# Kernel optimization log

Hardware: AMD Instinct MI355X
Metric: run time of the kernel (lower is better)

## Reference

```python
import jax, jax.numpy as jnp
import numpy as np

B = 64      # graphs in data1 batch
K = 50      # SortAggregation k
NPG = 1600  # nodes per graph in data1 (equal-size, contiguous batch vector)


def gcn_layer(x, src, dst, ew, W, b):
    # PyG GCNConv with edge_weight: add self loops (weight 1), symmetric norm.
    n = x.shape[0]
    idx = jnp.arange(n)
    src2 = jnp.concatenate([src, idx])
    dst2 = jnp.concatenate([dst, idx])
    ew2 = jnp.concatenate([ew, jnp.ones((n,), x.dtype)])
    deg = jax.ops.segment_sum(ew2, dst2, num_segments=n)
    dinv = jnp.where(deg > 0, jax.lax.rsqrt(deg), 0.0)
    norm = dinv[src2] * ew2 * dinv[dst2]
    h = x @ W                                   # [n, out]
    out = jax.ops.segment_sum(h[src2] * norm[:, None], dst2, num_segments=n)
    return out + b


def gnn(x, ei, ew, Wg1, bg1, Wg2, bg2):
    src, dst = ei[0], ei[1]
    h = jax.nn.relu(gcn_layer(x, src, dst, ew, Wg1, bg1))
    return jax.nn.relu(gcn_layer(h, src, dst, ew, Wg2, bg2))


def layer_norm(x, g, b, eps=1e-5):
    m = jnp.mean(x, -1, keepdims=True)
    v = jnp.mean((x - m) ** 2, -1, keepdims=True)
    return (x - m) * jax.lax.rsqrt(v + eps) * g + b


def setup_inputs() -> dict:
    key = jax.random.key(0)
    ks = jax.random.split(key, 16)
    N1, N2, F, E1, E2 = B * NPG, 199, 128, 1638400, 3184
    s = 0.05
    inp = {}
    inp["x1"] = jax.random.normal(ks[0], (N1, F), jnp.float32)
    inp["edge_attr1"] = jax.random.uniform(ks[1], (E1,), jnp.float32)
    inp["x2"] = jax.random.normal(ks[2], (N2, F), jnp.float32)
    inp["edge_attr2"] = jax.random.uniform(ks[3], (E2,), jnp.float32)
    inp["Wg1"] = jax.random.normal(ks[4], (F, 128), jnp.float32) * s
    inp["bg1"] = jnp.zeros((128,), jnp.float32)
    inp["Wg2"] = jax.random.normal(ks[5], (128, 64), jnp.float32) * s
    inp["bg2"] = jnp.zeros((64,), jnp.float32)
    inp["fc1_W"] = jax.random.normal(ks[6], (K * N2, 128), jnp.float32) * s
    inp["fc1_b"] = jnp.zeros((128,), jnp.float32)
    inp["ln1_g"] = jnp.ones((128,), jnp.float32)
    inp["ln1_b"] = jnp.zeros((128,), jnp.float32)
    inp["fc2_W"] = jax.random.normal(ks[7], (128, 64), jnp.float32) * s
    inp["fc2_b"] = jnp.zeros((64,), jnp.float32)
    inp["ln2_g"] = jnp.ones((64,), jnp.float32)
    inp["ln2_b"] = jnp.zeros((64,), jnp.float32)
    inp["fc3_W"] = jax.random.normal(ks[8], (64, 1), jnp.float32) * s
    inp["fc3_b"] = jnp.zeros((1,), jnp.float32)
    inp["edge_index1"] = jax.random.randint(ks[9], (2, E1), 0, N1)
    inp["edge_index2"] = jax.random.randint(ks[10], (2, E2), 0, N2)
    inp["batch1"] = jnp.repeat(jnp.arange(B), NPG)
    return inp


def reference(x1, edge_attr1, x2, edge_attr2, Wg1, bg1, Wg2, bg2,
              fc1_W, fc1_b, ln1_g, ln1_b, fc2_W, fc2_b, ln2_g, ln2_b,
              fc3_W, fc3_b, edge_index1, edge_index2, batch1):
    o1 = gnn(x1, edge_index1, edge_attr1, Wg1, bg1, Wg2, bg2)   # [N1, 64]
    o2 = gnn(x2, edge_index2, edge_attr2, Wg1, bg1, Wg2, bg2)   # [N2, 64]
    # torch.cdist(p=2) via gram trick (stable sqrt)
    d2 = (jnp.sum(o1 * o1, 1)[:, None] + jnp.sum(o2 * o2, 1)[None, :]
          - 2.0 * (o1 @ o2.T))
    dist = jnp.sqrt(jnp.maximum(d2, 0.0) + 1e-12)               # [N1, N2]
    # SortAggregation: batch1 is contiguous with equal-size graphs -> reshape
    dense = dist.reshape(B, NPG, -1)                            # [B, NPG, N2]
    _, idx = jax.lax.top_k(dense[:, :, -1], K)   # sort desc by last channel
    pooled = jnp.take_along_axis(dense, idx[:, :, None], axis=1)  # [B, K, N2]
    h = pooled.reshape(B, -1) @ fc1_W + fc1_b                   # [B, 128]
    h = jax.nn.relu(layer_norm(h, ln1_g, ln1_b))
    h = jax.nn.relu(layer_norm(h @ fc2_W + fc2_b, ln2_g, ln2_b))
    return jax.nn.sigmoid(h @ fc3_W + fc3_b)                    # [B, 1]
```

## Files before the change

### kernel.cpp

```cpp
#include <hip/hip_runtime.h>
#include <hip/hip_bf16.h>
#include <cstdint>


__device__ __forceinline__ int rfl(int v) { return __builtin_amdgcn_readfirstlane(v); }

__device__ __forceinline__ unsigned short f2bf(float f) {
    unsigned u = __float_as_uint(f);
    u = (u + 0x7fffu + ((u >> 16) & 1u)) >> 16;
    return (unsigned short)u;
}
__device__ __forceinline__ float lo16(unsigned v) { return __uint_as_float(v << 16); }
__device__ __forceinline__ float hi16(unsigned v) { return __uint_as_float(v & 0xffff0000u); }

#define BSHIFT 7
#define BNODES 128
#define BCAP 3072
#define XPAD 65

__global__ void bhist_kernel(const int* __restrict__ dst, int* bcnt, int E, int nbuk) {
    __shared__ int bins[832];
    int t = threadIdx.x;
    for (int i = t; i < nbuk; i += 256) bins[i] = 0;
    __syncthreads();
    for (int e = blockIdx.x * 256 + t; e < E; e += gridDim.x * 256)
        atomicAdd(&bins[dst[e] >> BSHIFT], 1);
    __syncthreads();
    for (int i = t; i < nbuk; i += 256) {
        int v = bins[i];
        if (v) atomicAdd(&bcnt[i], v);
    }
}

__global__ void bscan_kernel(const int* __restrict__ bcnt, int* __restrict__ boff,
                             int* __restrict__ bcur, int* __restrict__ off,
                             int nbuk, int E, int N1) {
    __shared__ int carry_s;
    int lane = threadIdx.x;
    if (lane == 0) carry_s = 0;
    __syncthreads();
    for (int base = 0; base < nbuk; base += 64) {
        int i = base + lane;
        int v = (i < nbuk) ? bcnt[i] : 0;
        int s = v;
        for (int d2 = 1; d2 < 64; d2 <<= 1) { int u = __shfl_up(s, d2); if (lane >= d2) s += u; }
        int c = carry_s;
        if (i < nbuk) { boff[i] = c + s - v; bcur[i] = c + s - v; }
        __syncthreads();
        if (lane == 63) carry_s = c + s;
        __syncthreads();
    }
    if (lane == 0) { boff[nbuk] = E; off[N1] = E; }
}

#define BP_EPB 16384
__global__ __launch_bounds__(1024) void bpart_kernel(const int* __restrict__ dst,
                                                     const int* __restrict__ src,
                                                     const float* __restrict__ ew,
                                                     int* bcur, int2* __restrict__ stag,
                                                     int E, int nbuk) {
    __shared__ int cnt[832];
    __shared__ int base[832];
    int t = threadIdx.x;
    int e0 = blockIdx.x * BP_EPB;
    for (int i = t; i < nbuk; i += 1024) cnt[i] = 0;
    __syncthreads();
#pragma unroll
    for (int k = 0; k < 16; k++) {
        int e = e0 + k * 1024 + t;
        if (e < E) atomicAdd(&cnt[dst[e] >> BSHIFT], 1);
    }
    __syncthreads();
    for (int i = t; i < nbuk; i += 1024) {
        int c = cnt[i];
        base[i] = c ? atomicAdd(&bcur[i], c) : 0;
    }
    __syncthreads();
    for (int i = t; i < nbuk; i += 1024) cnt[i] = 0;
    __syncthreads();
#pragma unroll
    for (int k = 0; k < 16; k++) {
        int e = e0 + k * 1024 + t;
        if (e < E) {
            int d = dst[e];
            int b = d >> BSHIFT, dl = d & (BNODES - 1);
            int l = atomicAdd(&cnt[b], 1);
            stag[base[b] + l] = make_int2((src[e] & 0xFFFFF) | (dl << 20),
                                          __float_as_int(ew[e]));
        }
    }
}

__global__ __launch_bounds__(256) void bfine_kernel(const int2* __restrict__ stag,
                                                    const int* __restrict__ boff,
                                                    int2* __restrict__ packed,
                                                    int* __restrict__ off,
                                                    float* __restrict__ dinv,
                                                    int nbuk, int N1) {
    __shared__ int2 ein[BCAP];
    __shared__ int2 eout[BCAP];
    __shared__ float ews[BNODES];
    __shared__ int hist[BNODES];
    __shared__ int sb[BNODES];
    __shared__ int cnt2[BNODES];
    int b = blockIdx.x, t = threadIdx.x;
    int base = boff[b], nE = boff[b + 1] - base;
    bool staged = (nE <= BCAP);
    if (t < BNODES) { hist[t] = 0; ews[t] = 0.f; cnt2[t] = 0; }
    __syncthreads();
    if (staged)
        for (int i = t; i < nE; i += 256) ein[i] = stag[base + i];
    __syncthreads();
    for (int i = t; i < nE; i += 256) {
        int2 m = staged ? ein[i] : stag[base + i];
        int dl = m.x >> 20;
        atomicAdd(&hist[dl], 1);
        atomicAdd(&ews[dl], __int_as_float(m.y));
    }
    __syncthreads();
    if (t < 64) {
        int v0 = hist[t]; int s0 = v0;
        for (int d2 = 1; d2 < 64; d2 <<= 1) { int u = __shfl_up(s0, d2); if (t >= d2) s0 += u; }
        sb[t] = s0 - v0;
        int tot0 = __shfl(s0, 63);
        int v1 = hist[64 + t]; int s1 = v1;
        for (int d2 = 1; d2 < 64; d2 <<= 1) { int u = __shfl_up(s1, d2); if (t >= d2) s1 += u; }
        sb[64 + t] = tot0 + s1 - v1;
    }
    __syncthreads();
    int node = b * BNODES + t;
    if (t < BNODES && node < N1) {
        off[node] = base + sb[t];
        dinv[node] = rsqrtf(1.0f + ews[t]);
    }
    __syncthreads();
    for (int i = t; i < nE; i += 256) {
        int2 m = staged ? ein[i] : stag[base + i];
        int dl = m.x >> 20;
        int l = atomicAdd(&cnt2[dl], 1);
        int2 o = make_int2(m.x & 0xFFFFF, m.y);
        if (staged) eout[sb[dl] + l] = o;
        else packed[base + sb[dl] + l] = o;
    }
    __syncthreads();
    if (staged)
        for (int i = t; i < nE; i += 256) packed[base + i] = eout[i];
}

__global__ __launch_bounds__(256) void gemm128_kernel(const float* __restrict__ x,
                                                      const float* __restrict__ w,
                                                      const float* __restrict__ dinv,
                                                      unsigned short* __restrict__ outb,
                                                      int nrows) {
    __shared__ float ws[64 * 128];
    __shared__ float xs[64 * XPAD];
    int t = threadIdx.x;
    size_t r0 = (size_t)blockIdx.x * 64;
    int tx = t % 16, ty = t / 16;
    float acc[4][8];
#pragma unroll
    for (int i = 0; i < 4; i++)
#pragma unroll
        for (int j = 0; j < 8; j++) acc[i][j] = 0.f;

    for (int half = 0; half < 2; half++) {
        __syncthreads();
        for (int f = t; f < 64 * 32; f += 256)
            ((float4*)ws)[f] = ((const float4*)(w + half * 64 * 128))[f];
        for (int f = t; f < 64 * 16; f += 256) {
            int row = f >> 4, c4 = f & 15;
            float4 v = *((const float4*)(x + (r0 + row) * 128 + half * 64 + c4 * 4));
            xs[row * XPAD + c4 * 4]     = v.x;
            xs[row * XPAD + c4 * 4 + 1] = v.y;
            xs[row * XPAD + c4 * 4 + 2] = v.z;
            xs[row * XPAD + c4 * 4 + 3] = v.w;
        }
        __syncthreads();
        for (int k = 0; k < 64; k++) {
            float4 b0 = *((const float4*)(ws + k * 128 + tx * 4));
            float4 b1 = *((const float4*)(ws + k * 128 + 64 + tx * 4));
            float bb[8] = {b0.x, b0.y, b0.z, b0.w, b1.x, b1.y, b1.z, b1.w};
#pragma unroll
            for (int i = 0; i < 4; i++) {
                float a = xs[(ty * 4 + i) * XPAD + k];
#pragma unroll
                for (int j = 0; j < 8; j++) acc[i][j] = fmaf(a, bb[j], acc[i][j]);
            }
        }
    }
#pragma unroll
    for (int i = 0; i < 4; i++) {
        size_t row = r0 + ty * 4 + i;
        float dv = dinv[row];
        uint2 pkA, pkB;
        pkA.x = (unsigned)f2bf(acc[i][0] * dv) | ((unsigned)f2bf(acc[i][1] * dv) << 16);
        pkA.y = (unsigned)f2bf(acc[i][2] * dv) | ((unsigned)f2bf(acc[i][3] * dv) << 16);
        pkB.x = (unsigned)f2bf(acc[i][4] * dv) | ((unsigned)f2bf(acc[i][5] * dv) << 16);
        pkB.y = (unsigned)f2bf(acc[i][6] * dv) | ((unsigned)f2bf(acc[i][7] * dv) << 16);
        *((uint2*)(outb + row * 128 + tx * 4)) = pkA;
        *((uint2*)(outb + row * 128 + 64 + tx * 4)) = pkB;
    }
}

__global__ __launch_bounds__(256) void gemm64b_kernel(const float* __restrict__ x,
                                                      const float* __restrict__ w,
                                                      const float* __restrict__ dinv,
                                                      unsigned short* __restrict__ outb,
                                                      int nrows) {
    __shared__ float ws[64 * 64];
    __shared__ float xs[64 * XPAD];
    int t = threadIdx.x;
    size_t r0 = (size_t)blockIdx.x * 64;
    int tx = t % 8, ty = t / 8;
    float acc[2][8];
#pragma unroll
    for (int i = 0; i < 2; i++)
#pragma unroll
        for (int j = 0; j < 8; j++) acc[i][j] = 0.f;

    for (int half = 0; half < 2; half++) {
        __syncthreads();
        for (int f = t; f < 64 * 16; f += 256)
            ((float4*)ws)[f] = ((const float4*)(w + half * 64 * 64))[f];
        for (int f = t; f < 64 * 16; f += 256) {
            int row = f >> 4, c4 = f & 15;
            float4 v = *((const float4*)(x + (r0 + row) * 128 + half * 64 + c4 * 4));
            xs[row * XPAD + c4 * 4]     = v.x;
            xs[row * XPAD + c4 * 4 + 1] = v.y;
            xs[row * XPAD + c4 * 4 + 2] = v.z;
            xs[row * XPAD + c4 * 4 + 3] = v.w;
        }
        __syncthreads();
        for (int k = 0; k < 64; k++) {
            float4 b0 = *((const float4*)(ws + k * 64 + tx * 4));
            float4 b1 = *((const float4*)(ws + k * 64 + 32 + tx * 4));
            float bb[8] = {b0.x, b0.y, b0.z, b0.w, b1.x, b1.y, b1.z, b1.w};
#pragma unroll
            for (int i = 0; i < 2; i++) {
                float a = xs[(ty * 2 + i) * XPAD + k];
#pragma unroll
                for (int j = 0; j < 8; j++) acc[i][j] = fmaf(a, bb[j], acc[i][j]);
            }
        }
    }
#pragma unroll
    for (int i = 0; i < 2; i++) {
        size_t row = r0 + ty * 2 + i;
        float dv = dinv[row];
        uint2 pk;
        pk.x = (unsigned)f2bf(acc[i][0] * dv) | ((unsigned)f2bf(acc[i][1] * dv) << 16);
        pk.y = (unsigned)f2bf(acc[i][2] * dv) | ((unsigned)f2bf(acc[i][3] * dv) << 16);
        *((uint2*)(outb + row * 64 + tx * 4)) = pk;
        pk.x = (unsigned)f2bf(acc[i][4] * dv) | ((unsigned)f2bf(acc[i][5] * dv) << 16);
        pk.y = (unsigned)f2bf(acc[i][6] * dv) | ((unsigned)f2bf(acc[i][7] * dv) << 16);
        *((uint2*)(outb + row * 64 + 32 + tx * 4)) = pk;
    }
}

__global__ __launch_bounds__(256) void agg128_kernel(const unsigned short* __restrict__ zs,
                                                     const int2* __restrict__ packed,
                                                     const int* __restrict__ off,
                                                     const float* __restrict__ dinv,
                                                     const float* __restrict__ bias,
                                                     float* __restrict__ h, int n) {
    int wid = threadIdx.x >> 6;
    int lane = threadIdx.x & 63;
    int d = rfl(blockIdx.x * 4 + wid);
    if (d >= n) return;
    const unsigned short* zl = zs + lane * 2;
    float dv = dinv[d];
    unsigned sv = *((const unsigned*)(zl + (size_t)d * 128));
    float acc0 = lo16(sv), acc1 = hi16(sv);
    float2 bv = *((const float2*)(bias + lane * 2));
    int e0 = off[d], e1 = off[d + 1];
    int e = e0;
    for (; e + 4 <= e1; e += 4) {
        int2 m0 = packed[e], m1 = packed[e + 1], m2 = packed[e + 2], m3 = packed[e + 3];
        int s0 = rfl(m0.x), s1 = rfl(m1.x), s2i = rfl(m2.x), s3 = rfl(m3.x);
        float w0 = __int_as_float(rfl(m0.y)), w1 = __int_as_float(rfl(m1.y));
        float w2v = __int_as_float(rfl(m2.y)), w3 = __int_as_float(rfl(m3.y));
        unsigned v0 = *((const unsigned*)(zl + (size_t)s0 * 128));
        unsigned v1 = *((const unsigned*)(zl + (size_t)s1 * 128));
        unsigned v2 = *((const unsigned*)(zl + (size_t)s2i * 128));
        unsigned v3 = *((const unsigned*)(zl + (size_t)s3 * 128));
        acc0 = fmaf(w0, lo16(v0), acc0); acc1 = fmaf(w0, hi16(v0), acc1);
        acc0 = fmaf(w1, lo16(v1), acc0); acc1 = fmaf(w1, hi16(v1), acc1);
        acc0 = fmaf(w2v, lo16(v2), acc0); acc1 = fmaf(w2v, hi16(v2), acc1);
        acc0 = fmaf(w3, lo16(v3), acc0); acc1 = fmaf(w3, hi16(v3), acc1);
    }
    for (; e < e1; e++) {
        int2 m = packed[e];
        int s = rfl(m.x);
        float w = __int_as_float(rfl(m.y));
        unsigned v = *((const unsigned*)(zl + (size_t)s * 128));
        acc0 = fmaf(w, lo16(v), acc0);
        acc1 = fmaf(w, hi16(v), acc1);
    }
    float2 hv = {fmaxf(dv * acc0 + bv.x, 0.f), fmaxf(dv * acc1 + bv.y, 0.f)};
    *((float2*)(h + (size_t)d * 128 + lane * 2)) = hv;
}

__global__ __launch_bounds__(256) void agg64_kernel(const unsigned short* __restrict__ zs2,
                                                    const int2* __restrict__ packed,
                                                    const int* __restrict__ off,
                                                    const float* __restrict__ dinv,
                                                    const float* __restrict__ bias,
                                                    float* __restrict__ o1buf, int n,
                                                    const float* __restrict__ o2,
                                                    const float* __restrict__ s2,
                                                    float* __restrict__ dlast, int N2) {
    int wid = threadIdx.x >> 6;
    int lane = threadIdx.x & 63;
    int d = rfl(blockIdx.x * 4 + wid);
    if (d >= n) return;
    const unsigned short* zl = zs2 + lane;
    float dv = dinv[d];
    float acc0 = __uint_as_float((unsigned)zl[(size_t)d * 64] << 16);
    float b0 = bias[lane];
    int e0 = off[d], e1 = off[d + 1];
    int e = e0;
    for (; e + 4 <= e1; e += 4) {
        int2 m0 = packed[e], m1 = packed[e + 1], m2 = packed[e + 2], m3 = packed[e + 3];
        int s0 = rfl(m0.x), s1 = rfl(m1.x), s2i = rfl(m2.x), s3 = rfl(m3.x);
        float w0 = __int_as_float(rfl(m0.y)), w1 = __int_as_float(rfl(m1.y));
        float w2v = __int_as_float(rfl(m2.y)), w3 = __int_as_float(rfl(m3.y));
        float v0 = __uint_as_float((unsigned)zl[(size_t)s0 * 64] << 16);
        float v1 = __uint_as_float((unsigned)zl[(size_t)s1 * 64] << 16);
        float v2 = __uint_as_float((unsigned)zl[(size_t)s2i * 64] << 16);
        float v3 = __uint_as_float((unsigned)zl[(size_t)s3 * 64] << 16);
        acc0 = fmaf(w0, v0, acc0);
        acc0 = fmaf(w1, v1, acc0);
        acc0 = fmaf(w2v, v2, acc0);
        acc0 = fmaf(w3, v3, acc0);
    }
    for (; e < e1; e++) {
        int2 m = packed[e];
        int s = rfl(m.x);
        float w = __int_as_float(rfl(m.y));
        acc0 = fmaf(w, __uint_as_float((unsigned)zl[(size_t)s * 64] << 16), acc0);
    }
    float a = fmaxf(dv * acc0 + b0, 0.f);
    o1buf[(size_t)d * 64 + lane] = a;
    float bl = o2[(size_t)(N2 - 1) * 64 + lane];
    float aa = a * a, ab = a * bl;
    for (int dd = 32; dd >= 1; dd >>= 1) {
        aa += __shfl_xor(aa, dd);
        ab += __shfl_xor(ab, dd);
    }
    if (lane == 0) {
        float d2 = aa + s2[N2 - 1] - 2.f * ab;
        dlast[d] = sqrtf(fmaxf(d2, 0.f) + 1e-12f);
    }
}

__global__ void g2_prep(const int* __restrict__ ei2, const float* __restrict__ ew2,
                        float* dinv2, float* a2a, float* a2b, int E2, int N2) {
    __shared__ float degl[256];
    int t = threadIdx.x;
    degl[t] = 1.0f;
    __syncthreads();
    for (int e = t; e < E2; e += 256) atomicAdd(&degl[ei2[E2 + e]], ew2[e]);
    __syncthreads();
    if (t < N2) dinv2[t] = rsqrtf(degl[t]);
    for (int i = t; i < N2 * 128; i += 256) a2a[i] = 0.f;
    for (int i = t; i < N2 * 64; i += 256) a2b[i] = 0.f;
}

template <int NCOL>
__global__ void g2_gemm(const float* __restrict__ x, const float* __restrict__ w,
                        float* __restrict__ z, int N2) {
    __shared__ float xr[128];
    int row = blockIdx.x, t = threadIdx.x;
    for (int k = t; k < 128; k += NCOL) xr[k] = x[row * 128 + k];
    __syncthreads();
    float acc = 0.f;
    for (int k = 0; k < 128; k++) acc = fmaf(xr[k], w[k * NCOL + t], acc);
    z[row * NCOL + t] = acc;
}

template <int C>
__global__ void g2_scatter(const float* __restrict__ z, const int* __restrict__ ei2,
                           const float* __restrict__ ew2, const float* __restrict__ dinv2,
                           float* a2, int E2) {
    constexpr int CPL = C / 64;
    int wid = threadIdx.x >> 6, lane = threadIdx.x & 63;
    int e = blockIdx.x * 4 + wid;
    if (e >= E2) return;
    int s = ei2[e], d = ei2[E2 + e];
    float nm = dinv2[s] * ew2[e] * dinv2[d];
#pragma unroll
    for (int q = 0; q < CPL; q++) {
        int c = lane * CPL + q;
        atomicAdd(&a2[d * C + c], nm * z[s * C + c]);
    }
}

__global__ void g2_fin128(const float* __restrict__ a2, const float* __restrict__ z,
                          const float* __restrict__ dinv2, const float* __restrict__ bias,
                          float* __restrict__ out, int N2) {
    int i = blockIdx.x * 256 + threadIdx.x;
    if (i >= N2 * 128) return;
    int n = i / 128, c = i % 128;
    float dv = dinv2[n];
    out[i] = fmaxf(a2[i] + dv * dv * z[i] + bias[c], 0.f);
}

__global__ void g2_fin64s2(const float* __restrict__ a2, const float* __restrict__ z,
                           const float* __restrict__ dinv2, const float* __restrict__ bias,
                           float* __restrict__ out, float* __restrict__ s2, int N2) {
    int wid = threadIdx.x >> 6, lane = threadIdx.x & 63;
    int row = blockIdx.x * 4 + wid;
    if (row >= N2) return;
    int i = row * 64 + lane;
    float dv = dinv2[row];
    float v = fmaxf(a2[i] + dv * dv * z[i] + bias[lane], 0.f);
    out[i] = v;
    float ss = v * v;
    for (int d = 32; d >= 1; d >>= 1) ss += __shfl_xor(ss, d);
    if (lane == 0) s2[row] = ss;
}

__global__ __launch_bounds__(256) void topk_kernel(const float* __restrict__ dlast,
                                                   int* __restrict__ topidx,
                                                   int NPG, int K) {
    __shared__ unsigned long long keys[1600];
    __shared__ unsigned long long wmax[4];
    int g = blockIdx.x, t = threadIdx.x;
    int lane = t & 63, wid = t >> 6;
    for (int r = t; r < NPG; r += 256) {
        unsigned vb = __float_as_uint(dlast[(size_t)g * NPG + r]);
        keys[r] = ((unsigned long long)vb << 32) | (unsigned)(NPG - 1 - r);
    }
    __syncthreads();
    for (int it = 0; it < K; it++) {
        unsigned long long m = 0ull;
        for (int r = t; r < NPG; r += 256) { unsigned long long k = keys[r]; if (k > m) m = k; }
        for (int d = 32; d >= 1; d >>= 1) {
            unsigned long long u = __shfl_xor(m, d);
            if (u > m) m = u;
        }
        if (lane == 0) wmax[wid] = m;
        __syncthreads();
        if (t == 0) {
            unsigned long long mm = wmax[0];
            for (int w = 1; w < 4; w++) if (wmax[w] > mm) mm = wmax[w];
            int rbest = NPG - 1 - (int)(mm & 0xffffffffull);
            topidx[g * K + it] = rbest;
            keys[rbest] = 0ull;
        }
        __syncthreads();
    }
}

__global__ void pooled_kernel(const float* __restrict__ o1, const float* __restrict__ o2,
                              const float* __restrict__ s2, const int* __restrict__ topidx,
                              float* __restrict__ pooled, int NPG, int K, int N2) {
    __shared__ float o1s[64];
    __shared__ float s1sh;
    int g = blockIdx.x / K, kk = blockIdx.x % K;
    int t = threadIdx.x;
    int r = topidx[g * K + kk];
    size_t node = (size_t)g * NPG + r;
    if (t < 64) o1s[t] = o1[node * 64 + t];
    __syncthreads();
    if (t < 64) {
        float v = o1s[t]; float ss = v * v;
        for (int d = 32; d >= 1; d >>= 1) ss += __shfl_xor(ss, d);
        if (t == 0) s1sh = ss;
    }
    __syncthreads();
    if (t < N2) {
        float dot = 0.f;
#pragma unroll 8
        for (int k2 = 0; k2 < 64; k2++) dot = fmaf(o1s[k2], o2[t * 64 + k2], dot);
        float d2 = s1sh + s2[t] - 2.f * dot;
        pooled[(size_t)blockIdx.x * N2 + t] = sqrtf(fmaxf(d2, 0.f) + 1e-12f);
    }
}

#define FC1_CH 32
__global__ __launch_bounds__(256) void fc1_kernel(const float* __restrict__ pooled,
                                                  const float* __restrict__ fc1W,
                                                  float* __restrict__ h1p,
                                                  int PK, int NCHUNK, int B) {
    __shared__ float ps[64][FC1_CH];
    int ch = blockIdx.x;
    int r0 = ch * FC1_CH;
    int nr = min(FC1_CH, PK - r0);
    int t = threadIdx.x;
    for (int f = t; f < 64 * FC1_CH; f += 256) {
        int b = f / FC1_CH, r = f % FC1_CH;
        ps[b][r] = (r < nr && b < B) ? pooled[(size_t)b * PK + r0 + r] : 0.f;
    }
    int c = t & 127, bh = t >> 7;
    float wreg[FC1_CH];
#pragma unroll
    for (int r = 0; r < FC1_CH; r++)
        wreg[r] = (r < nr) ? fc1W[(size_t)(r0 + r) * 128 + c] : 0.f;
    __syncthreads();
    for (int bb = 0; bb < 32; bb++) {
        int b = bh * 32 + bb;
        float acc = 0.f;
#pragma unroll
        for (int r = 0; r < FC1_CH; r++) acc = fmaf(ps[b][r], wreg[r], acc);
        if (b < B) h1p[((size_t)b * NCHUNK + ch) * 128 + c] = acc;
    }
}

__global__ __launch_bounds__(256) void fc1red_kernel(const float* __restrict__ h1p,
                                                     const float* __restrict__ fc1b,
                                                     float* __restrict__ h1full,
                                                     int NCHUNK, int B) {
    int wid = threadIdx.x >> 6, lane = threadIdx.x & 63;
    int o = blockIdx.x * 4 + wid;
    if (o >= B * 128) return;
    int b = o >> 7, c = o & 127;
    float s = 0.f;
    for (int ch = lane; ch < NCHUNK; ch += 64)
        s += h1p[((size_t)b * NCHUNK + ch) * 128 + c];
    for (int dd = 32; dd >= 1; dd >>= 1) s += __shfl_xor(s, dd);
    if (lane == 0) h1full[o] = s + fc1b[c];
}

__global__ __launch_bounds__(256) void head2_kernel(
    const float* __restrict__ h1full,
    const float* __restrict__ ln1g, const float* __restrict__ ln1b,
    const float* __restrict__ fc2W, const float* __restrict__ fc2b,
    const float* __restrict__ ln2g, const float* __restrict__ ln2b,
    const float* __restrict__ fc3W, const float* __restrict__ fc3b,
    float* __restrict__ out) {
    __shared__ float red[256];
    __shared__ float h1[128];
    __shared__ float h2[64];
    int b = blockIdx.x, t = threadIdx.x;
    if (t < 128) h1[t] = h1full[b * 128 + t];
    __syncthreads();
    red[t] = (t < 128) ? h1[t] : 0.f;
    __syncthreads();
    for (int s = 128; s >= 1; s >>= 1) { if (t < s) red[t] += red[t + s]; __syncthreads(); }
    float mean1 = red[0] / 128.f;
    __syncthreads();
    float dv1 = (t < 128) ? (h1[t] - mean1) : 0.f;
    red[t] = dv1 * dv1;
    __syncthreads();
    for (int s = 128; s >= 1; s >>= 1) { if (t < s) red[t] += red[t + s]; __syncthreads(); }
    float var1 = red[0] / 128.f;
    __syncthreads();
    if (t < 128) {
        float y = (h1[t] - mean1) * rsqrtf(var1 + 1e-5f) * ln1g[t] + ln1b[t];
        h1[t] = fmaxf(y, 0.f);
    }
    __syncthreads();
    if (t < 64) {
        float a2v = 0.f;
        for (int k2 = 0; k2 < 128; k2++) a2v = fmaf(h1[k2], fc2W[k2 * 64 + t], a2v);
        h2[t] = a2v + fc2b[t];
    }
    __syncthreads();
    red[t] = (t < 64) ? h2[t] : 0.f;
    __syncthreads();
    for (int s = 128; s >= 1; s >>= 1) { if (t < s) red[t] += red[t + s]; __syncthreads(); }
    float mean2 = red[0] / 64.f;
    __syncthreads();
    float dv2 = (t < 64) ? (h2[t] - mean2) : 0.f;
    red[t] = dv2 * dv2;
    __syncthreads();
    for (int s = 128; s >= 1; s >>= 1) { if (t < s) red[t] += red[t + s]; __syncthreads(); }
    float var2 = red[0] / 64.f;
    __syncthreads();
    if (t < 64)
        h2[t] = fmaxf((h2[t] - mean2) * rsqrtf(var2 + 1e-5f) * ln2g[t] + ln2b[t], 0.f);
    __syncthreads();
    red[t] = (t < 64) ? h2[t] * fc3W[t] : 0.f;
    __syncthreads();
    for (int s = 128; s >= 1; s >>= 1) { if (t < s) red[t] += red[t + s]; __syncthreads(); }
    if (t == 0) out[b] = 1.f / (1.f + expf(-(red[0] + fc3b[0])));
}

extern "C" void kernel_launch(void* const* d_in, const int* in_sizes, int n_in,
                              void* d_out, int out_size, void* d_ws, size_t ws_size,
                              hipStream_t stream) {
    const float* x1   = (const float*)d_in[0];
    const float* ew1  = (const float*)d_in[1];
    const float* x2   = (const float*)d_in[2];
    const float* ew2  = (const float*)d_in[3];
    const float* Wg1  = (const float*)d_in[4];
    const float* bg1  = (const float*)d_in[5];
    const float* Wg2  = (const float*)d_in[6];
    const float* bg2  = (const float*)d_in[7];
    const float* fc1W = (const float*)d_in[8];
    const float* fc1b = (const float*)d_in[9];
    const float* ln1g = (const float*)d_in[10];
    const float* ln1b = (const float*)d_in[11];
    const float* fc2W = (const float*)d_in[12];
    const float* fc2b = (const float*)d_in[13];
    const float* ln2g = (const float*)d_in[14];
    const float* ln2b = (const float*)d_in[15];
    const float* fc3W = (const float*)d_in[16];
    const float* fc3b = (const float*)d_in[17];
    const int* ei1    = (const int*)d_in[18];
    const int* ei2    = (const int*)d_in[19];
    float* out = (float*)d_out;

    const int N1 = in_sizes[0] / 128;
    const int E1 = in_sizes[1];
    const int N2 = in_sizes[2] / 128;
    const int E2 = in_sizes[3];
    const int B  = out_size;
    const int NPG = N1 / B;
    const int K  = (in_sizes[8] / 128) / N2;
    const int PK = K * N2;
    const int NCHUNK = (PK + FC1_CH - 1) / FC1_CH;
    const int NBUK = (N1 + BNODES - 1) / BNODES;

    char* wsb = (char*)d_ws;
    size_t o = 0;
    auto alloc = [&](size_t bytes) -> void* {
        void* p = wsb + o;
        o += (bytes + 255) & ~(size_t)255;
        return p;
    };
    int*   bcnt   = (int*)alloc((size_t)NBUK * 4);
    int*   boff   = (int*)alloc((size_t)(NBUK + 1) * 4);
    int*   bcur   = (int*)alloc((size_t)NBUK * 4);
    int2*  stag   = (int2*)alloc((size_t)E1 * 8);
    int2*  packed = (int2*)alloc((size_t)E1 * 8);
    int*   off    = (int*)alloc((size_t)(N1 + 1) * 4);
    float* dinv1  = (float*)alloc((size_t)N1 * 4);
    unsigned short* zs1 = (unsigned short*)alloc((size_t)N1 * 128 * 2);
    float* h      = (float*)alloc((size_t)N1 * 128 * 4);
    unsigned short* zs2 = (unsigned short*)alloc((size_t)N1 * 64 * 2);
    float* o1buf  = (float*)alloc((size_t)N1 * 64 * 4);
    float* dl     = (float*)alloc((size_t)N1 * 4);
    int*   tki    = (int*)alloc((size_t)B * K * 4);
    float* pooled = (float*)alloc((size_t)B * K * N2 * 4);
    float* h1p    = (float*)alloc((size_t)B * NCHUNK * 128 * 4);
    float* h1full = (float*)alloc((size_t)B * 128 * 4);
    float* dinv2  = (float*)alloc((size_t)N2 * 4);
    float* z2g    = (float*)alloc((size_t)N2 * 128 * 4);
    float* h2b    = (float*)alloc((size_t)N2 * 128 * 4);
    float* a2a    = (float*)alloc((size_t)N2 * 128 * 4);
    float* zz2    = (float*)alloc((size_t)N2 * 64 * 4);
    float* a2b    = (float*)alloc((size_t)N2 * 64 * 4);
    float* o2b    = (float*)alloc((size_t)N2 * 64 * 4);
    float* s2     = (float*)alloc((size_t)N2 * 4);
    (void)ws_size; (void)n_in;

    const int* src1 = ei1;
    const int* dst1 = ei1 + E1;

    hipMemsetAsync(bcnt, 0, (size_t)NBUK * 4, stream);
    bhist_kernel<<<400, 256, 0, stream>>>(dst1, bcnt, E1, NBUK);
    bscan_kernel<<<1, 64, 0, stream>>>(bcnt, boff, bcur, off, NBUK, E1, N1);
    bpart_kernel<<<(E1 + BP_EPB - 1) / BP_EPB, 1024, 0, stream>>>(dst1, src1, ew1, bcur,
                                                                  stag, E1, NBUK);
    bfine_kernel<<<NBUK, 256, 0, stream>>>(stag, boff, packed, off, dinv1, NBUK, N1);

    gemm128_kernel<<<N1 / 64, 256, 0, stream>>>(x1, Wg1, dinv1, zs1, N1);
    agg128_kernel<<<N1 / 4, 256, 0, stream>>>(zs1, packed, off, dinv1, bg1, h, N1);
    gemm64b_kernel<<<N1 / 64, 256, 0, stream>>>(h, Wg2, dinv1, zs2, N1);

    g2_prep<<<1, 256, 0, stream>>>(ei2, ew2, dinv2, a2a, a2b, E2, N2);
    g2_gemm<128><<<N2, 128, 0, stream>>>(x2, Wg1, z2g, N2);
    g2_scatter<128><<<(E2 + 3) / 4, 256, 0, stream>>>(z2g, ei2, ew2, dinv2, a2a, E2);
    g2_fin128<<<(N2 * 128 + 255) / 256, 256, 0, stream>>>(a2a, z2g, dinv2, bg1, h2b, N2);
    g2_gemm<64><<<N2, 64, 0, stream>>>(h2b, Wg2, zz2, N2);
    g2_scatter<64><<<(E2 + 3) / 4, 256, 0, stream>>>(zz2, ei2, ew2, dinv2, a2b, E2);
    g2_fin64s2<<<(N2 + 3) / 4, 256, 0, stream>>>(a2b, zz2, dinv2, bg2, o2b, s2, N2);

    agg64_kernel<<<N1 / 4, 256, 0, stream>>>(zs2, packed, off, dinv1, bg2, o1buf, N1,
                                             o2b, s2, dl, N2);

    topk_kernel<<<B, 256, 0, stream>>>(dl, tki, NPG, K);
    pooled_kernel<<<B * K, 256, 0, stream>>>(o1buf, o2b, s2, tki, pooled, NPG, K, N2);
    fc1_kernel<<<NCHUNK, 256, 0, stream>>>(pooled, fc1W, h1p, PK, NCHUNK, B);
    fc1red_kernel<<<(B * 128 + 3) / 4, 256, 0, stream>>>(h1p, fc1b, h1full, NCHUNK, B);
    head2_kernel<<<B, 256, 0, stream>>>(h1full, ln1g, ln1b, fc2W, fc2b,
                                        ln2g, ln2b, fc3W, fc3b, out);
}
```

Baseline: 418.7 us.

## Slice first-layer features into 16-column planes for cache-local aggregation

The first GEMM now writes its bf16 output in eight column-sliced planes of 16 features each. A new aggregation kernel processes one slice per block, with each wave handling 8 edges at a time through lane groups plus a shuffle reduction. The hidden activations are stored in the same sliced layout and the second GEMM reads them that way. The intent is to shrink each slice's gather working set so random neighbor reads hit in cache more often, at the cost of 8x more blocks and repeated reads of the edge lists per slice.

New measurement: 632.4 us. 51.1% more time.

```diff
diff --git a/kernel.cpp b/kernel.cpp
--- a/kernel.cpp
+++ b/kernel.cpp
@@ -188,6 +188,7 @@
             }
         }
     }
+    int sliceA = tx >> 2, offc = (tx * 4) & 15;
 #pragma unroll
     for (int i = 0; i < 4; i++) {
         size_t row = r0 + ty * 4 + i;
@@ -197,8 +198,48 @@
         pkA.y = (unsigned)f2bf(acc[i][2] * dv) | ((unsigned)f2bf(acc[i][3] * dv) << 16);
         pkB.x = (unsigned)f2bf(acc[i][4] * dv) | ((unsigned)f2bf(acc[i][5] * dv) << 16);
         pkB.y = (unsigned)f2bf(acc[i][6] * dv) | ((unsigned)f2bf(acc[i][7] * dv) << 16);
-        *((uint2*)(outb + row * 128 + tx * 4)) = pkA;
-        *((uint2*)(outb + row * 128 + 64 + tx * 4)) = pkB;
+        *((uint2*)(outb + (size_t)sliceA * nrows * 16 + row * 16 + offc)) = pkA;
+        *((uint2*)(outb + (size_t)(4 + sliceA) * nrows * 16 + row * 16 + offc)) = pkB;
+    }
+}
+
+__global__ __launch_bounds__(256) void agg128s_kernel(const unsigned short* __restrict__ zs,
+                                                      const int2* __restrict__ packed,
+                                                      const int* __restrict__ off,
+                                                      const float* __restrict__ dinv,
+                                                      const float* __restrict__ bias,
+                                                      float* __restrict__ h, int n) {
+    int wid = threadIdx.x >> 6;
+    int lane = threadIdx.x & 63;
+    int slice = blockIdx.x & 7;
+    int d = rfl((blockIdx.x >> 3) * 4 + wid);
+    if (d >= n) return;
+    const unsigned short* zsl = zs + (size_t)slice * n * 16;
+    int g = lane >> 3, c = lane & 7;
+    float dv = dinv[d];
+    unsigned vd = *((const unsigned*)(zsl + (size_t)d * 16 + c * 2));
+    float acc0 = (g == 0) ? lo16(vd) : 0.f;
+    float acc1 = (g == 0) ? hi16(vd) : 0.f;
+    int e0 = off[d], e1 = off[d + 1];
+    for (int e = e0; e < e1; e += 8) {
+        int2 mr = make_int2(d, 0);
+        if (lane < 8) {
+            int ee = e + lane;
+            if (ee < e1) mr = packed[ee];
+        }
+        int sp = __shfl(mr.x, g);
+        float wp = __int_as_float(__shfl(mr.y, g));
+        unsigned v = *((const unsigned*)(zsl + (size_t)sp * 16 + c * 2));
+        acc0 = fmaf(wp, lo16(v), acc0);
+        acc1 = fmaf(wp, hi16(v), acc1);
+    }
+    acc0 += __shfl_xor(acc0, 8);  acc1 += __shfl_xor(acc1, 8);
+    acc0 += __shfl_xor(acc0, 16); acc1 += __shfl_xor(acc1, 16);
+    acc0 += __shfl_xor(acc0, 32); acc1 += __shfl_xor(acc1, 32);
+    if (lane < 8) {
+        float2 bv = *((const float2*)(bias + slice * 16 + c * 2));
+        float2 hv = {fmaxf(dv * acc0 + bv.x, 0.f), fmaxf(dv * acc1 + bv.y, 0.f)};
+        *((float2*)(h + (size_t)slice * n * 16 + (size_t)d * 16 + c * 2)) = hv;
     }
 }
 
@@ -224,7 +265,9 @@
             ((float4*)ws)[f] = ((const float4*)(w + half * 64 * 64))[f];
         for (int f = t; f < 64 * 16; f += 256) {
             int row = f >> 4, c4 = f & 15;
-            float4 v = *((const float4*)(x + (r0 + row) * 128 + half * 64 + c4 * 4));
+            int col0 = half * 64 + c4 * 4;
+            float4 v = *((const float4*)(x + (size_t)(col0 >> 4) * nrows * 16 +
+                                         (r0 + row) * 16 + (col0 & 15)));
             xs[row * XPAD + c4 * 4]     = v.x;
             xs[row * XPAD + c4 * 4 + 1] = v.y;
             xs[row * XPAD + c4 * 4 + 2] = v.z;
@@ -255,49 +298,6 @@
         pk.y = (unsigned)f2bf(acc[i][6] * dv) | ((unsigned)f2bf(acc[i][7] * dv) << 16);
         *((uint2*)(outb + row * 64 + 32 + tx * 4)) = pk;
     }
-}
-
-__global__ __launch_bounds__(256) void agg128_kernel(const unsigned short* __restrict__ zs,
-                                                     const int2* __restrict__ packed,
-                                                     const int* __restrict__ off,
-                                                     const float* __restrict__ dinv,
-                                                     const float* __restrict__ bias,
-                                                     float* __restrict__ h, int n) {
-    int wid = threadIdx.x >> 6;
-    int lane = threadIdx.x & 63;
-    int d = rfl(blockIdx.x * 4 + wid);
-    if (d >= n) return;
-    const unsigned short* zl = zs + lane * 2;
-    float dv = dinv[d];
-    unsigned sv = *((const unsigned*)(zl + (size_t)d * 128));
-    float acc0 = lo16(sv), acc1 = hi16(sv);
-    float2 bv = *((const float2*)(bias + lane * 2));
-    int e0 = off[d], e1 = off[d + 1];
-    int e = e0;
-    for (; e + 4 <= e1; e += 4) {
-        int2 m0 = packed[e], m1 = packed[e + 1], m2 = packed[e + 2], m3 = packed[e + 3];
-        int s0 = rfl(m0.x), s1 = rfl(m1.x), s2i = rfl(m2.x), s3 = rfl(m3.x);
-        float w0 = __int_as_float(rfl(m0.y)), w1 = __int_as_float(rfl(m1.y));
-        float w2v = __int_as_float(rfl(m2.y)), w3 = __int_as_float(rfl(m3.y));
-        unsigned v0 = *((const unsigned*)(zl + (size_t)s0 * 128));
-        unsigned v1 = *((const unsigned*)(zl + (size_t)s1 * 128));
-        unsigned v2 = *((const unsigned*)(zl + (size_t)s2i * 128));
-        unsigned v3 = *((const unsigned*)(zl + (size_t)s3 * 128));
-        acc0 = fmaf(w0, lo16(v0), acc0); acc1 = fmaf(w0, hi16(v0), acc1);
-        acc0 = fmaf(w1, lo16(v1), acc0); acc1 = fmaf(w1, hi16(v1), acc1);
-        acc0 = fmaf(w2v, lo16(v2), acc0); acc1 = fmaf(w2v, hi16(v2), acc1);
-        acc0 = fmaf(w3, lo16(v3), acc0); acc1 = fmaf(w3, hi16(v3), acc1);
-    }
-    for (; e < e1; e++) {
-        int2 m = packed[e];
-        int s = rfl(m.x);
-        float w = __int_as_float(rfl(m.y));
-        unsigned v = *((const unsigned*)(zl + (size_t)s * 128));
-        acc0 = fmaf(w, lo16(v), acc0);
-        acc1 = fmaf(w, hi16(v), acc1);
-    }
-    float2 hv = {fmaxf(dv * acc0 + bv.x, 0.f), fmaxf(dv * acc1 + bv.y, 0.f)};
-    *((float2*)(h + (size_t)d * 128 + lane * 2)) = hv;
 }
 
 __global__ __launch_bounds__(256) void agg64_kernel(const unsigned short* __restrict__ zs2,
@@ -657,7 +657,7 @@
     bfine_kernel<<<NBUK, 256, 0, stream>>>(stag, boff, packed, off, dinv1, NBUK, N1);
 
     gemm128_kernel<<<N1 / 64, 256, 0, stream>>>(x1, Wg1, dinv1, zs1, N1);
-    agg128_kernel<<<N1 / 4, 256, 0, stream>>>(zs1, packed, off, dinv1, bg1, h, N1);
+    agg128s_kernel<<<(N1 / 4) * 8, 256, 0, stream>>>(zs1, packed, off, dinv1, bg1, h, N1);
     gemm64b_kernel<<<N1 / 64, 256, 0, stream>>>(h, Wg2, dinv1, zs2, N1);
 
     g2_prep<<<1, 256, 0, stream>>>(ei2, ew2, dinv2, a2a, a2b, E2, N2);
```
